# Kernel optimization log

Hardware: AMD Instinct MI355X
Metric: run time of the kernel (lower is better)

## Reference

```python
import jax, jax.numpy as jnp
import numpy as np

D_MODEL = 1024
NUM_HEADS = 16
D_HEAD = D_MODEL // NUM_HEADS
LN_EPS = 1e-5


def setup_inputs() -> dict:
    key = jax.random.key(0)
    ks = jax.random.split(key, 10)
    s = 1.0 / np.sqrt(D_MODEL)
    inp = {
        "batch": jax.random.normal(ks[0], (4, 2048, D_MODEL), dtype=jnp.float32),
        "wq": jax.random.uniform(ks[1], (D_MODEL, D_MODEL), jnp.float32, -s, s),
        "bq": jax.random.uniform(ks[2], (D_MODEL,), jnp.float32, -s, s),
        "wk": jax.random.uniform(ks[3], (D_MODEL, D_MODEL), jnp.float32, -s, s),
        "bk": jax.random.uniform(ks[4], (D_MODEL,), jnp.float32, -s, s),
        "wv": jax.random.uniform(ks[5], (D_MODEL, D_MODEL), jnp.float32, -s, s),
        "bv": jax.random.uniform(ks[6], (D_MODEL,), jnp.float32, -s, s),
        "wo": jax.random.uniform(ks[7], (D_MODEL, D_MODEL), jnp.float32, -s, s),
        "bo": jax.random.uniform(ks[8], (D_MODEL,), jnp.float32, -s, s),
        "ln_g": jnp.ones((D_MODEL,), jnp.float32),
        "ln_b": jnp.zeros((D_MODEL,), jnp.float32),
    }
    return inp


def reference(batch, wq, bq, wk, bk, wv, bv, wo, bo, ln_g, ln_b):
    B, S, D = batch.shape
    # QKV projections (torch Linear: x @ W.T + b)
    q = (batch @ wq.T + bq).reshape(B, S, NUM_HEADS, D_HEAD)
    k = (batch @ wk.T + bk).reshape(B, S, NUM_HEADS, D_HEAD)
    v = (batch @ wv.T + bv).reshape(B, S, NUM_HEADS, D_HEAD)
    # attention scores [B, H, S, S]
    scores = jnp.einsum("bqhd,bkhd->bhqk", q, k) / np.sqrt(D_HEAD).astype(np.float32)
    # (original masked_fill is not in-place -> mask has no effect; omitted)
    probs = jax.nn.softmax(scores, axis=-1)
    attn = jnp.einsum("bhqk,bkhd->bqhd", probs, v).reshape(B, S, D)
    residual = attn @ wo.T + bo  # dropout = identity (eval mode)
    x = batch + residual
    mu = jnp.mean(x, axis=-1, keepdims=True)
    var = jnp.mean(jnp.square(x - mu), axis=-1, keepdims=True)
    return (x - mu) / jnp.sqrt(var + LN_EPS) * ln_g + ln_b
```

## Files before the change

### kernel.cpp

```cpp
#include <hip/hip_runtime.h>

typedef __bf16 bf16_t;
typedef __bf16 v8bf __attribute__((ext_vector_type(8)));
typedef __bf16 v4bf __attribute__((ext_vector_type(4)));
typedef float  v4f  __attribute__((ext_vector_type(4)));

#define D_MODEL 1024
#define NHEAD   16
#define DHEAD   64
#define SEQ     2048
#define BATCH   4
#define ROWS    (BATCH*SEQ)

#define GLD16(g, l) __builtin_amdgcn_global_load_lds( \
    (const __attribute__((address_space(1))) void*)(g), \
    (__attribute__((address_space(3))) void*)(l), 16, 0, 0)

__global__ __launch_bounds__(256) void k_prep(const float* __restrict__ batch,
                                              const float* __restrict__ wq,
                                              const float* __restrict__ wk,
                                              const float* __restrict__ wv,
                                              const float* __restrict__ wo,
                                              const float* __restrict__ bq,
                                              const float* __restrict__ bk,
                                              const float* __restrict__ bv,
                                              bf16_t* __restrict__ Xb,
                                              bf16_t* __restrict__ Wqkv,
                                              bf16_t* __restrict__ Wob,
                                              float* __restrict__ bqkv) {
    int bid = blockIdx.x, t = threadIdx.x;
    const float* src; bf16_t* dst; int idx;
    if (bid < 8192)       { src = batch; dst = Xb;             idx = bid * 256 + t; }
    else if (bid < 9216)  { src = wq;    dst = Wqkv;           idx = (bid - 8192) * 256 + t; }
    else if (bid < 10240) { src = wk;    dst = Wqkv + 1048576; idx = (bid - 9216) * 256 + t; }
    else if (bid < 11264) { src = wv;    dst = Wqkv + 2097152; idx = (bid - 10240) * 256 + t; }
    else if (bid < 12288) { src = wo;    dst = Wob;            idx = (bid - 11264) * 256 + t; }
    else {
        int i = (bid - 12288) * 256 + t;
        if (i < 1024) bqkv[i] = bq[i];
        else if (i < 2048) bqkv[i] = bk[i - 1024];
        else if (i < 3072) bqkv[i] = bv[i - 2048];
        return;
    }
    float4 f = ((const float4*)src)[idx];
    v4bf o;
    o[0] = (bf16_t)f.x; o[1] = (bf16_t)f.y; o[2] = (bf16_t)f.z; o[3] = (bf16_t)f.w;
    ((v4bf*)dst)[idx] = o;
}

__global__ __launch_bounds__(256, 3) void k_gemm_bt(
    const bf16_t* __restrict__ A, const bf16_t* __restrict__ Bm,
    const float* __restrict__ bias, const float* __restrict__ resid,
    bf16_t* __restrict__ Cb, float* __restrict__ Cf,
    int M, int N, int K, int qcols, float qmul)
{
    __shared__ bf16_t As[3][128 * 32];
    __shared__ bf16_t Bs[3][128 * 32];

    int nTile = N >> 7;
    int x = blockIdx.x & 7, g = blockIdx.x >> 3;
    int n_idx = g % nTile;
    int m_idx = (g / nTile) * 8 + x;
    int m0 = m_idx << 7;
    int n0 = n_idx << 7;
    int t = threadIdx.x;
    int w = t >> 6, lane = t & 63, quad = lane >> 4, ln = lane & 15;
    int wm = (w >> 1) << 6, wn = (w & 1) << 6;

    int srow = lane >> 2;
    int scol = ((lane & 3) ^ ((lane >> 3) & 3)) << 3;
    const bf16_t* Ag0 = A  + (size_t)(m0 + w * 16 +      srow) * K + scol;
    const bf16_t* Ag1 = A  + (size_t)(m0 + w * 16 + 64 + srow) * K + scol;
    const bf16_t* Bg0 = Bm + (size_t)(n0 + w * 16 +      srow) * K + scol;
    const bf16_t* Bg1 = Bm + (size_t)(n0 + w * 16 + 64 + srow) * K + scol;
    int lo0 = (w * 16) * 32, lo1 = (w * 16 + 64) * 32;

    v4f acc[4][4];
#pragma unroll
    for (int i = 0; i < 4; i++)
#pragma unroll
        for (int j = 0; j < 4; j++) acc[i][j] = (v4f){0.f, 0.f, 0.f, 0.f};

    bf16_t* aPrev = As[2]; bf16_t* aCur = As[0]; bf16_t* aNext = As[1];
    bf16_t* bPrev = Bs[2]; bf16_t* bCur = Bs[0]; bf16_t* bNext = Bs[1];

    GLD16(Ag0, aCur + lo0);
    GLD16(Ag1, aCur + lo1);
    GLD16(Bg0, bCur + lo0);
    GLD16(Bg1, bCur + lo1);
    GLD16(Ag0 + 32, aNext + lo0);
    GLD16(Ag1 + 32, aNext + lo1);
    GLD16(Bg0 + 32, bNext + lo0);
    GLD16(Bg1 + 32, bNext + lo1);

    int sw = (ln >> 1) & 3;
    for (int k0 = 0; k0 < K; k0 += 32) {
        if (k0 + 32 < K) asm volatile("s_waitcnt vmcnt(4)" ::: "memory");
        else             asm volatile("s_waitcnt vmcnt(0)" ::: "memory");
        __builtin_amdgcn_s_barrier();
        __builtin_amdgcn_sched_barrier(0);
        if (k0 + 64 < K) {
            GLD16(Ag0 + k0 + 64, aPrev + lo0);
            GLD16(Ag1 + k0 + 64, aPrev + lo1);
            GLD16(Bg0 + k0 + 64, bPrev + lo0);
            GLD16(Bg1 + k0 + 64, bPrev + lo1);
        }
        v8bf af[4], bfr[4];
#pragma unroll
        for (int mt = 0; mt < 4; mt++)
            af[mt] = *(const v8bf*)&aCur[(wm + mt * 16 + ln) * 32 + ((quad ^ sw) << 3)];
#pragma unroll
        for (int nt = 0; nt < 4; nt++)
            bfr[nt] = *(const v8bf*)&bCur[(wn + nt * 16 + ln) * 32 + ((quad ^ sw) << 3)];
#pragma unroll
        for (int mt = 0; mt < 4; mt++)
#pragma unroll
            for (int nt = 0; nt < 4; nt++)
                acc[mt][nt] = __builtin_amdgcn_mfma_f32_16x16x32_bf16(af[mt], bfr[nt], acc[mt][nt], 0, 0, 0);
        bf16_t* ta = aPrev; aPrev = aCur; aCur = aNext; aNext = ta;
        bf16_t* tb = bPrev; bPrev = bCur; bCur = bNext; bNext = tb;
    }

#pragma unroll
    for (int mt = 0; mt < 4; mt++) {
#pragma unroll
        for (int r = 0; r < 4; r++) {
            int row = m0 + wm + mt * 16 + quad * 4 + r;
#pragma unroll
            for (int nt = 0; nt < 4; nt++) {
                int col = n0 + wn + nt * 16 + ln;
                float v = acc[mt][nt][r] + bias[col];
                if (Cf) Cf[(size_t)row * N + col] = v + resid[(size_t)row * N + col];
                else {
                    if (col < qcols) v *= qmul;
                    Cb[(size_t)row * N + col] = (bf16_t)v;
                }
            }
        }
    }
}

__global__ __launch_bounds__(256) void k_transpose_v(const bf16_t* __restrict__ qkv,
                                                     bf16_t* __restrict__ vt) {
    __shared__ bf16_t tile[64 * 72];
    int bid = blockIdx.x;
    int st = bid & 31, bh = bid >> 5, b = bh >> 4, h = bh & 15;
    int t = threadIdx.x;
    const bf16_t* src = qkv + (size_t)(b * SEQ + st * 64) * 3072 + 2048 + h * 64;
#pragma unroll
    for (int i = 0; i < 2; i++) {
        int c = t + i * 256, row = c >> 3, c8 = (c & 7) << 3;
        *(uint4*)&tile[row * 72 + c8] = *(const uint4*)(src + (size_t)row * 3072 + c8);
    }
    __syncthreads();
    bf16_t* dst = vt + (size_t)bh * DHEAD * SEQ + st * 64;
#pragma unroll
    for (int i = 0; i < 2; i++) {
        int c = t + i * 256, d = c >> 3, s8 = (c & 7) << 3;
        v8bf o;
#pragma unroll
        for (int j = 0; j < 8; j++) o[j] = tile[(s8 + j) * 72 + d];
        *(v8bf*)(dst + (size_t)d * SEQ + s8) = o;
    }
}

__global__ __launch_bounds__(256, 2) void k_attn(const bf16_t* __restrict__ qkv,
                                                 const bf16_t* __restrict__ vt,
                                                 bf16_t* __restrict__ attn) {
    __shared__ bf16_t Ks[2][64 * 64];
    __shared__ bf16_t Vs[2][64 * 64];

    int bid = blockIdx.x;
    int xcd = bid & 7, g = bid >> 3;
    int qt = g & 15;
    int bh = ((g >> 4) << 3) | xcd;
    int b = bh >> 4, h = bh & 15;
    int t = threadIdx.x, w = t >> 6, lane = t & 63, quad = lane >> 4, ln = lane & 15;
    int q0 = qt * 128 + w * 32;

    v8bf qf[2][2];
#pragma unroll
    for (int qs = 0; qs < 2; qs++) {
        const bf16_t* Qp = qkv + (size_t)(b * SEQ + q0 + qs * 16 + ln) * 3072 + h * 64 + quad * 8;
        qf[qs][0] = *(const v8bf*)Qp;
        qf[qs][1] = *(const v8bf*)(Qp + 32);
    }

    int srow = lane >> 3;
    int scol = ((lane & 7) ^ ((lane >> 3) & 3) ^ ((w & 1) << 2)) << 3;
    const bf16_t* Kg0 = qkv + (size_t)(b * SEQ + w * 8 +      srow) * 3072 + 1024 + h * 64 + scol;
    const bf16_t* Kg1 = qkv + (size_t)(b * SEQ + w * 8 + 32 + srow) * 3072 + 1024 + h * 64 + scol;
    const bf16_t* Vg0 = vt + (size_t)bh * DHEAD * SEQ + (size_t)(w * 8 +      srow) * SEQ + scol;
    const bf16_t* Vg1 = vt + (size_t)bh * DHEAD * SEQ + (size_t)(w * 8 + 32 + srow) * SEQ + scol;
    int ko0 = (w * 8) * 64, ko1 = (w * 8 + 32) * 64;

    int gk = (ln & 3) | (((ln >> 2) & 1) << 2);
    int gv = (ln & 3) | (((ln >> 3) & 1) << 2);
    int rrbase = ((ln >> 2) << 3) + (ln & 3);
    int o0 = (rrbase) * 64,       o1 = (rrbase + 4) * 64;
    int o2 = (rrbase + 32) * 64,  o3 = (rrbase + 36) * 64;

    const v4f z4 = (v4f){0.f, 0.f, 0.f, 0.f};
    v8bf ones8;
#pragma unroll
    for (int j = 0; j < 8; j++) ones8[j] = (bf16_t)1.0f;

    v4f o[2][4];
#pragma unroll
    for (int qs = 0; qs < 2; qs++)
#pragma unroll
        for (int d = 0; d < 4; d++) o[qs][d] = z4;
    v4f den[2] = {z4, z4};

    GLD16(Kg0, &Ks[0][ko0]);
    GLD16(Kg1, &Ks[0][ko1]);
    GLD16(Vg0, &Vs[0][ko0]);
    GLD16(Vg1, &Vs[0][ko1]);

    int buf = 0;
    for (int kt = 0; kt < SEQ; kt += 64, buf ^= 1) {
        __syncthreads();
        if (kt + 64 < SEQ) {
            GLD16(Kg0 + (size_t)(kt + 64) * 3072, &Ks[buf ^ 1][ko0]);
            GLD16(Kg1 + (size_t)(kt + 64) * 3072, &Ks[buf ^ 1][ko1]);
            GLD16(Vg0 + kt + 64, &Vs[buf ^ 1][ko0]);
            GLD16(Vg1 + kt + 64, &Vs[buf ^ 1][ko1]);
        }

        const bf16_t* Kb = &Ks[buf][0];
        v4f s0[4], s1[4];
        int rof[4] = {o0, o1, o2, o3};
#pragma unroll
        for (int nt = 0; nt < 4; nt++) {
            v8bf kf0 = *(const v8bf*)&Kb[rof[nt] + ((quad ^ gk) << 3)];
            v8bf kf1 = *(const v8bf*)&Kb[rof[nt] + (((quad | 4) ^ gk) << 3)];
            s0[nt] = __builtin_amdgcn_mfma_f32_16x16x32_bf16(kf0, qf[0][0], z4, 0, 0, 0);
            s0[nt] = __builtin_amdgcn_mfma_f32_16x16x32_bf16(kf1, qf[0][1], s0[nt], 0, 0, 0);
            s1[nt] = __builtin_amdgcn_mfma_f32_16x16x32_bf16(kf0, qf[1][0], z4, 0, 0, 0);
            s1[nt] = __builtin_amdgcn_mfma_f32_16x16x32_bf16(kf1, qf[1][1], s1[nt], 0, 0, 0);
        }

#pragma unroll
        for (int tk = 0; tk < 2; tk++) {
            v8bf vfd[4];
#pragma unroll
            for (int d = 0; d < 4; d++)
                vfd[d] = *(const v8bf*)&Vs[buf][(d * 16 + ln) * 64 + (((tk * 4 + quad) ^ gv) << 3)];
#pragma unroll
            for (int qs = 0; qs < 2; qs++) {
                v4f* s = qs ? s1 : s0;
                float e0 = __builtin_amdgcn_exp2f(s[2 * tk][0]);
                float e1 = __builtin_amdgcn_exp2f(s[2 * tk][1]);
                float e2 = __builtin_amdgcn_exp2f(s[2 * tk][2]);
                float e3 = __builtin_amdgcn_exp2f(s[2 * tk][3]);
                float e4 = __builtin_amdgcn_exp2f(s[2 * tk + 1][0]);
                float e5 = __builtin_amdgcn_exp2f(s[2 * tk + 1][1]);
                float e6 = __builtin_amdgcn_exp2f(s[2 * tk + 1][2]);
                float e7 = __builtin_amdgcn_exp2f(s[2 * tk + 1][3]);
                v8bf pf;
                pf[0] = (bf16_t)e0; pf[1] = (bf16_t)e1; pf[2] = (bf16_t)e2; pf[3] = (bf16_t)e3;
                pf[4] = (bf16_t)e4; pf[5] = (bf16_t)e5; pf[6] = (bf16_t)e6; pf[7] = (bf16_t)e7;
                den[qs] = __builtin_amdgcn_mfma_f32_16x16x32_bf16(pf, ones8, den[qs], 0, 0, 0);
#pragma unroll
                for (int d = 0; d < 4; d++)
                    o[qs][d] = __builtin_amdgcn_mfma_f32_16x16x32_bf16(pf, vfd[d], o[qs][d], 0, 0, 0);
            }
        }
    }

#pragma unroll
    for (int qs = 0; qs < 2; qs++) {
        int rowg = b * SEQ + q0 + qs * 16;
#pragma unroll
        for (int r = 0; r < 4; r++) {
            float inv = 1.f / den[qs][r];
#pragma unroll
            for (int d = 0; d < 4; d++)
                attn[(size_t)(rowg + quad * 4 + r) * D_MODEL + h * 64 + d * 16 + ln] =
                    (bf16_t)(o[qs][d][r] * inv);
        }
    }
}

__global__ __launch_bounds__(256) void k_layernorm(const float* __restrict__ y,
                                                   const float* __restrict__ g,
                                                   const float* __restrict__ beta,
                                                   float* __restrict__ out) {
    __shared__ float rs[4], rq[4];
    int row = blockIdx.x, t = threadIdx.x;
    int w = t >> 6, lane = t & 63;
    float4 v = ((const float4*)(y + (size_t)row * D_MODEL))[t];
    float s = v.x + v.y + v.z + v.w;
    float q = v.x * v.x + v.y * v.y + v.z * v.z + v.w * v.w;
#pragma unroll
    for (int off = 1; off < 64; off <<= 1) {
        s += __shfl_xor(s, off);
        q += __shfl_xor(q, off);
    }
    if (lane == 0) { rs[w] = s; rq[w] = q; }
    __syncthreads();
    s = rs[0] + rs[1] + rs[2] + rs[3];
    q = rq[0] + rq[1] + rq[2] + rq[3];
    float mu = s * (1.f / D_MODEL);
    float var = q * (1.f / D_MODEL) - mu * mu;
    float rstd = rsqrtf(var + 1e-5f);
    float4 gg = ((const float4*)g)[t];
    float4 bb = ((const float4*)beta)[t];
    float4 o;
    o.x = (v.x - mu) * rstd * gg.x + bb.x;
    o.y = (v.y - mu) * rstd * gg.y + bb.y;
    o.z = (v.z - mu) * rstd * gg.z + bb.z;
    o.w = (v.w - mu) * rstd * gg.w + bb.w;
    ((float4*)(out + (size_t)row * D_MODEL))[t] = o;
}

extern "C" void kernel_launch(void* const* d_in, const int* in_sizes, int n_in,
                              void* d_out, int out_size, void* d_ws, size_t ws_size,
                              hipStream_t stream) {
    const float* batch = (const float*)d_in[0];
    const float* wq = (const float*)d_in[1];
    const float* bq = (const float*)d_in[2];
    const float* wk = (const float*)d_in[3];
    const float* bk = (const float*)d_in[4];
    const float* wv = (const float*)d_in[5];
    const float* bv = (const float*)d_in[6];
    const float* wo = (const float*)d_in[7];
    const float* bo = (const float*)d_in[8];
    const float* ln_g = (const float*)d_in[9];
    const float* ln_b = (const float*)d_in[10];
    float* out = (float*)d_out;

    char* ws = (char*)d_ws;
    size_t offXb   = 0;
    size_t offWqkv = offXb + (size_t)ROWS * D_MODEL * 2;
    size_t offWo   = offWqkv + (size_t)3072 * 1024 * 2;
    size_t offBias = offWo + (size_t)1024 * 1024 * 2;
    size_t offQKV  = offBias + 3072 * 4;
    size_t offAttn = offQKV + (size_t)ROWS * 3072 * 2;
    size_t total   = offAttn + (size_t)ROWS * D_MODEL * 2;
    if (ws_size < total) return;

    bf16_t* Xb   = (bf16_t*)(ws + offXb);
    bf16_t* Vt   = (bf16_t*)(ws + offXb);
    bf16_t* Wqkv = (bf16_t*)(ws + offWqkv);
    bf16_t* Wob  = (bf16_t*)(ws + offWo);
    float*  bqkv = (float*)(ws + offBias);
    bf16_t* qkv  = (bf16_t*)(ws + offQKV);
    float*  y    = (float*)(ws + offQKV);
    bf16_t* attn = (bf16_t*)(ws + offAttn);

    const float SC = 0.125f * 1.44269504088896f;

    k_prep<<<12300, 256, 0, stream>>>(batch, wq, wk, wv, wo, bq, bk, bv,
                                      Xb, Wqkv, Wob, bqkv);
    k_gemm_bt<<<64 * 24, 256, 0, stream>>>(Xb, Wqkv, bqkv, nullptr, qkv, nullptr,
                                           8192, 3072, 1024, 1024, SC);
    k_transpose_v<<<2048, 256, 0, stream>>>(qkv, Vt);
    k_attn<<<1024, 256, 0, stream>>>(qkv, Vt, attn);
    k_gemm_bt<<<64 * 8, 256, 0, stream>>>(attn, Wob, bo, batch, nullptr, y,
                                          8192, 1024, 1024, 0, 1.0f);
    k_layernorm<<<8192, 256, 0, stream>>>(y, ln_g, ln_b, out);
}
```

Baseline: 298.4 us.

## Use 256x256-tile 8-wave pipelined GEMM for QKV projection

Replaces the 128x128-tile QKV GEMM with a dedicated 512-thread kernel that computes 256x256 output tiles. It uses double-buffered LDS split into K-halves, direct global-to-LDS loads with manual vmcnt waits and barriers, and s_setprio around the MFMA bursts. The block index is also remapped so blocks are grouped for L2 reuse. The aim is more operand reuse per LDS byte and better overlap of loads with MFMA. In exchange it has far more accumulator registers per thread, only 384 blocks, and a fragile hand-written wait schedule.

```diff
diff --git a/kernel.cpp b/kernel.cpp
--- a/kernel.cpp
+++ b/kernel.cpp
@@ -15,6 +15,15 @@
 #define GLD16(g, l) __builtin_amdgcn_global_load_lds( \
     (const __attribute__((address_space(1))) void*)(g), \
     (__attribute__((address_space(3))) void*)(l), 16, 0, 0)
+
+#define BAR asm volatile("s_barrier" ::: "memory")
+#define VW8 asm volatile("s_waitcnt vmcnt(8)" ::: "memory")
+#define VW4 asm volatile("s_waitcnt vmcnt(4)" ::: "memory")
+#define VW0 asm volatile("s_waitcnt vmcnt(0)" ::: "memory")
+#define TB   BAR
+#define TW8  do { VW8; BAR; } while(0)
+#define TW4  do { VW4; BAR; } while(0)
+#define TW0  do { VW0; BAR; } while(0)
 
 __global__ __launch_bounds__(256) void k_prep(const float* __restrict__ batch,
                                               const float* __restrict__ wq,
@@ -48,6 +57,131 @@
     ((v4bf*)dst)[idx] = o;
 }
 
+__global__ __launch_bounds__(512, 2) void k_gemm256(
+    const bf16_t* __restrict__ A, const bf16_t* __restrict__ Bm,
+    const float* __restrict__ bias, bf16_t* __restrict__ C, float qmul)
+{
+    __shared__ bf16_t As[2][2][256 * 32];
+    __shared__ bf16_t Bs[2][2][256 * 32];
+
+    const int K = 1024;
+    int bid = blockIdx.x;
+    int wg = (bid & 7) * 48 + (bid >> 3);
+    int m_idx = wg / 12, n_idx = wg % 12;
+    int m0 = m_idx << 8, n0 = n_idx << 8;
+
+    int t = threadIdx.x;
+    int lane = t & 63, quad = lane >> 4, ln = lane & 15;
+    int w = t >> 6, wr = w >> 2, wc = w & 3;
+
+    int cl = (t & 3) ^ ((t >> 2) & 3);
+    const bf16_t* Ag = A  + (size_t)(m0 + (t >> 2)) * K + cl * 8;
+    const bf16_t* Bg = Bm + (size_t)(n0 + (t >> 2)) * K + cl * 8;
+    int wb = (t >> 6) << 9;
+
+#define STA_(bufv, khv, kc) do { const bf16_t* g_ = Ag + (kc) + ((khv) << 5); \
+    GLD16(g_, &As[bufv][khv][wb]); GLD16(g_ + 131072, &As[bufv][khv][wb + 4096]); } while(0)
+#define STB_(bufv, khv, kc) do { const bf16_t* g_ = Bg + (kc) + ((khv) << 5); \
+    GLD16(g_, &Bs[bufv][khv][wb]); GLD16(g_ + 131072, &Bs[bufv][khv][wb + 4096]); } while(0)
+
+    int rsw = (quad ^ (ln & 3)) << 3;
+    int aof = (wr * 128 + ln) * 32 + rsw;
+    int bof = (wc * 64 + ln) * 32 + rsw;
+
+    v4f acc[8][4];
+#pragma unroll
+    for (int i = 0; i < 8; i++)
+#pragma unroll
+        for (int j = 0; j < 4; j++) acc[i][j] = (v4f){0.f, 0.f, 0.f, 0.f};
+
+    v8bf bfr[4];
+
+#define MFMA16(M0) \
+    acc[(M0)+0][0] = __builtin_amdgcn_mfma_f32_16x16x32_bf16(a0_, bfr[0], acc[(M0)+0][0], 0, 0, 0); \
+    acc[(M0)+0][1] = __builtin_amdgcn_mfma_f32_16x16x32_bf16(a0_, bfr[1], acc[(M0)+0][1], 0, 0, 0); \
+    acc[(M0)+0][2] = __builtin_amdgcn_mfma_f32_16x16x32_bf16(a0_, bfr[2], acc[(M0)+0][2], 0, 0, 0); \
+    acc[(M0)+0][3] = __builtin_amdgcn_mfma_f32_16x16x32_bf16(a0_, bfr[3], acc[(M0)+0][3], 0, 0, 0); \
+    acc[(M0)+1][0] = __builtin_amdgcn_mfma_f32_16x16x32_bf16(a1_, bfr[0], acc[(M0)+1][0], 0, 0, 0); \
+    acc[(M0)+1][1] = __builtin_amdgcn_mfma_f32_16x16x32_bf16(a1_, bfr[1], acc[(M0)+1][1], 0, 0, 0); \
+    acc[(M0)+1][2] = __builtin_amdgcn_mfma_f32_16x16x32_bf16(a1_, bfr[2], acc[(M0)+1][2], 0, 0, 0); \
+    acc[(M0)+1][3] = __builtin_amdgcn_mfma_f32_16x16x32_bf16(a1_, bfr[3], acc[(M0)+1][3], 0, 0, 0); \
+    acc[(M0)+2][0] = __builtin_amdgcn_mfma_f32_16x16x32_bf16(a2_, bfr[0], acc[(M0)+2][0], 0, 0, 0); \
+    acc[(M0)+2][1] = __builtin_amdgcn_mfma_f32_16x16x32_bf16(a2_, bfr[1], acc[(M0)+2][1], 0, 0, 0); \
+    acc[(M0)+2][2] = __builtin_amdgcn_mfma_f32_16x16x32_bf16(a2_, bfr[2], acc[(M0)+2][2], 0, 0, 0); \
+    acc[(M0)+2][3] = __builtin_amdgcn_mfma_f32_16x16x32_bf16(a2_, bfr[3], acc[(M0)+2][3], 0, 0, 0); \
+    acc[(M0)+3][0] = __builtin_amdgcn_mfma_f32_16x16x32_bf16(a3_, bfr[0], acc[(M0)+3][0], 0, 0, 0); \
+    acc[(M0)+3][1] = __builtin_amdgcn_mfma_f32_16x16x32_bf16(a3_, bfr[1], acc[(M0)+3][1], 0, 0, 0); \
+    acc[(M0)+3][2] = __builtin_amdgcn_mfma_f32_16x16x32_bf16(a3_, bfr[2], acc[(M0)+3][2], 0, 0, 0); \
+    acc[(M0)+3][3] = __builtin_amdgcn_mfma_f32_16x16x32_bf16(a3_, bfr[3], acc[(M0)+3][3], 0, 0, 0);
+
+#define PHASE(bufv, khv, mhv, STAGE, TAIL) do { \
+    const bf16_t* Ab_ = &As[bufv][khv][0]; \
+    if (!(mhv)) { \
+        const bf16_t* Bb_ = &Bs[bufv][khv][0]; \
+        bfr[0] = *(const v8bf*)&Bb_[bof]; \
+        bfr[1] = *(const v8bf*)&Bb_[bof + 512]; \
+        bfr[2] = *(const v8bf*)&Bb_[bof + 1024]; \
+        bfr[3] = *(const v8bf*)&Bb_[bof + 1536]; \
+    } \
+    v8bf a0_ = *(const v8bf*)&Ab_[aof + ((mhv) * 4 + 0) * 512]; \
+    v8bf a1_ = *(const v8bf*)&Ab_[aof + ((mhv) * 4 + 1) * 512]; \
+    v8bf a2_ = *(const v8bf*)&Ab_[aof + ((mhv) * 4 + 2) * 512]; \
+    v8bf a3_ = *(const v8bf*)&Ab_[aof + ((mhv) * 4 + 3) * 512]; \
+    STAGE; \
+    BAR; \
+    __builtin_amdgcn_s_setprio(1); \
+    MFMA16((mhv) * 4); \
+    __builtin_amdgcn_s_setprio(0); \
+    TAIL; \
+} while(0)
+
+    STA_(0, 0, 0); STB_(0, 0, 0);
+    STA_(0, 1, 0); STB_(0, 1, 0);
+    STA_(1, 0, 64); STB_(1, 0, 64);
+    VW8; BAR;
+
+    int kb = 0;
+#pragma unroll 1
+    for (int tp = 0; tp < 7; ++tp, kb += 128) {
+        PHASE(0, 0, 0, STA_(1, 1, kb + 64),  TB);
+        PHASE(0, 0, 1, STB_(1, 1, kb + 64),  TW8);
+        PHASE(0, 1, 0, STA_(0, 0, kb + 128), TB);
+        PHASE(0, 1, 1, STB_(0, 0, kb + 128), TW8);
+        PHASE(1, 0, 0, STA_(0, 1, kb + 128), TB);
+        PHASE(1, 0, 1, STB_(0, 1, kb + 128), TW8);
+        PHASE(1, 1, 0, STA_(1, 0, kb + 192), TB);
+        PHASE(1, 1, 1, STB_(1, 0, kb + 192), TW8);
+    }
+    PHASE(0, 0, 0, STA_(1, 1, 960), TB);
+    PHASE(0, 0, 1, STB_(1, 1, 960), TW8);
+    PHASE(0, 1, 0, ((void)0),       TB);
+    PHASE(0, 1, 1, ((void)0),       TW4);
+    PHASE(1, 0, 0, ((void)0), TB);
+    PHASE(1, 0, 1, ((void)0), TW0);
+    PHASE(1, 1, 0, ((void)0), TB);
+    PHASE(1, 1, 1, ((void)0), TB);
+
+#undef PHASE
+#undef MFMA16
+#undef STA_
+#undef STB_
+
+#pragma unroll
+    for (int m = 0; m < 8; m++) {
+#pragma unroll
+        for (int r = 0; r < 4; r++) {
+            int row = m0 + wr * 128 + m * 16 + quad * 4 + r;
+#pragma unroll
+            for (int n = 0; n < 4; n++) {
+                int col = n0 + wc * 64 + n * 16 + ln;
+                float v = acc[m][n][r] + bias[col];
+                if (col < 1024) v *= qmul;
+                C[(size_t)row * 3072 + col] = (bf16_t)v;
+            }
+        }
+    }
+}
+
 __global__ __launch_bounds__(256, 3) void k_gemm_bt(
     const bf16_t* __restrict__ A, const bf16_t* __restrict__ Bm,
     const float* __restrict__ bias, const float* __restrict__ resid,
@@ -353,8 +487,7 @@
 
     k_prep<<<12300, 256, 0, stream>>>(batch, wq, wk, wv, wo, bq, bk, bv,
                                       Xb, Wqkv, Wob, bqkv);
-    k_gemm_bt<<<64 * 24, 256, 0, stream>>>(Xb, Wqkv, bqkv, nullptr, qkv, nullptr,
-                                           8192, 3072, 1024, 1024, SC);
+    k_gemm256<<<384, 512, 0, stream>>>(Xb, Wqkv, bqkv, qkv, SC);
     k_transpose_v<<<2048, 256, 0, stream>>>(qkv, Vt);
     k_attn<<<1024, 256, 0, stream>>>(qkv, Vt, attn);
     k_gemm_bt<<<64 * 8, 256, 0, stream>>>(attn, Wob, bo, batch, nullptr, y,
```

New measurement: 303.1 us. Within noise of the previous version (+1.6%).

## Use 128x256 tile GEMM for QKV projection and re-swizzle V LDS layout

Applied to the files above, without the earlier changes.

Adds a new GEMM kernel with 128x256 output tiles (each wave computes 64x128) and an XCD-aware block mapping, used for the fused QKV projection. The wider tile raises arithmetic intensity and cuts re-reads of A from global memory, but uses more accumulator registers and LDS, so occupancy drops to 2 blocks per CU. The attention kernel also switches to a different XOR swizzle for V tiles in LDS, which is meant to reduce bank conflicts on the V reads. The epilogue writes scalar bf16 stores, which are less coalesced than vector stores.

```diff
diff --git a/kernel.cpp b/kernel.cpp
--- a/kernel.cpp
+++ b/kernel.cpp
@@ -48,6 +48,98 @@
     ((v4bf*)dst)[idx] = o;
 }
 
+__global__ __launch_bounds__(256, 2) void k_gemm_bt2(
+    const bf16_t* __restrict__ A, const bf16_t* __restrict__ Bm,
+    const float* __restrict__ bias, bf16_t* __restrict__ Cb,
+    int M, int N, int K, int qcols, float qmul)
+{
+    __shared__ bf16_t As[3][128 * 32];
+    __shared__ bf16_t Bs[3][256 * 32];
+
+    int nT = N >> 8;
+    int cpx = ((M >> 7) * nT) >> 3;
+    int bid = blockIdx.x;
+    int wg = (bid & 7) * cpx + (bid >> 3);
+    int m_idx = wg / nT, n_idx = wg % nT;
+    int m0 = m_idx << 7, n0 = n_idx << 8;
+
+    int t = threadIdx.x;
+    int w = t >> 6, lane = t & 63, quad = lane >> 4, ln = lane & 15;
+    int wm = (w >> 1) << 6, wn = (w & 1) << 7;
+
+    int srow = lane >> 2;
+    int scol = ((lane & 3) ^ ((lane >> 3) & 3)) << 3;
+    const bf16_t* Ag0 = A  + (size_t)(m0 + w * 16 + srow) * K + scol;
+    const bf16_t* Ag1 = Ag0 + (size_t)64 * K;
+    const bf16_t* Bg0 = Bm + (size_t)(n0 + w * 16 + srow) * K + scol;
+    const bf16_t* Bg1 = Bg0 + (size_t)64 * K;
+    const bf16_t* Bg2 = Bg0 + (size_t)128 * K;
+    const bf16_t* Bg3 = Bg0 + (size_t)192 * K;
+    int la0 = (w * 16) * 32, la1 = (w * 16 + 64) * 32;
+    int lb0 = (w * 16) * 32;
+
+    v4f acc[4][8];
+#pragma unroll
+    for (int i = 0; i < 4; i++)
+#pragma unroll
+        for (int j = 0; j < 8; j++) acc[i][j] = (v4f){0.f, 0.f, 0.f, 0.f};
+
+    bf16_t* aPrev = As[2]; bf16_t* aCur = As[0]; bf16_t* aNext = As[1];
+    bf16_t* bPrev = Bs[2]; bf16_t* bCur = Bs[0]; bf16_t* bNext = Bs[1];
+
+    GLD16(Ag0, aCur + la0); GLD16(Ag1, aCur + la1);
+    GLD16(Bg0, bCur + lb0); GLD16(Bg1, bCur + lb0 + 2048);
+    GLD16(Bg2, bCur + lb0 + 4096); GLD16(Bg3, bCur + lb0 + 6144);
+    GLD16(Ag0 + 32, aNext + la0); GLD16(Ag1 + 32, aNext + la1);
+    GLD16(Bg0 + 32, bNext + lb0); GLD16(Bg1 + 32, bNext + lb0 + 2048);
+    GLD16(Bg2 + 32, bNext + lb0 + 4096); GLD16(Bg3 + 32, bNext + lb0 + 6144);
+
+    int rsw = (quad ^ ((ln >> 1) & 3)) << 3;
+    for (int k0 = 0; k0 < K; k0 += 32) {
+        if (k0 + 32 < K) asm volatile("s_waitcnt vmcnt(6)" ::: "memory");
+        else             asm volatile("s_waitcnt vmcnt(0)" ::: "memory");
+        __builtin_amdgcn_s_barrier();
+        __builtin_amdgcn_sched_barrier(0);
+        if (k0 + 64 < K) {
+            GLD16(Ag0 + k0 + 64, aPrev + la0);
+            GLD16(Ag1 + k0 + 64, aPrev + la1);
+            GLD16(Bg0 + k0 + 64, bPrev + lb0);
+            GLD16(Bg1 + k0 + 64, bPrev + lb0 + 2048);
+            GLD16(Bg2 + k0 + 64, bPrev + lb0 + 4096);
+            GLD16(Bg3 + k0 + 64, bPrev + lb0 + 6144);
+        }
+        v8bf af[4], bfr[8];
+#pragma unroll
+        for (int mt = 0; mt < 4; mt++)
+            af[mt] = *(const v8bf*)&aCur[(wm + mt * 16 + ln) * 32 + rsw];
+#pragma unroll
+        for (int nt = 0; nt < 8; nt++)
+            bfr[nt] = *(const v8bf*)&bCur[(wn + nt * 16 + ln) * 32 + rsw];
+#pragma unroll
+        for (int mt = 0; mt < 4; mt++)
+#pragma unroll
+            for (int nt = 0; nt < 8; nt++)
+                acc[mt][nt] = __builtin_amdgcn_mfma_f32_16x16x32_bf16(af[mt], bfr[nt], acc[mt][nt], 0, 0, 0);
+        bf16_t* ta = aPrev; aPrev = aCur; aCur = aNext; aNext = ta;
+        bf16_t* tb = bPrev; bPrev = bCur; bCur = bNext; bNext = tb;
+    }
+
+#pragma unroll
+    for (int mt = 0; mt < 4; mt++) {
+#pragma unroll
+        for (int r = 0; r < 4; r++) {
+            int row = m0 + wm + mt * 16 + quad * 4 + r;
+#pragma unroll
+            for (int nt = 0; nt < 8; nt++) {
+                int col = n0 + wn + nt * 16 + ln;
+                float v = acc[mt][nt][r] + bias[col];
+                if (col < qcols) v *= qmul;
+                Cb[(size_t)row * N + col] = (bf16_t)v;
+            }
+        }
+    }
+}
+
 __global__ __launch_bounds__(256, 3) void k_gemm_bt(
     const bf16_t* __restrict__ A, const bf16_t* __restrict__ Bm,
     const float* __restrict__ bias, const float* __restrict__ resid,
@@ -187,15 +279,16 @@
     }
 
     int srow = lane >> 3;
-    int scol = ((lane & 7) ^ ((lane >> 3) & 3) ^ ((w & 1) << 2)) << 3;
-    const bf16_t* Kg0 = qkv + (size_t)(b * SEQ + w * 8 +      srow) * 3072 + 1024 + h * 64 + scol;
-    const bf16_t* Kg1 = qkv + (size_t)(b * SEQ + w * 8 + 32 + srow) * 3072 + 1024 + h * 64 + scol;
-    const bf16_t* Vg0 = vt + (size_t)bh * DHEAD * SEQ + (size_t)(w * 8 +      srow) * SEQ + scol;
-    const bf16_t* Vg1 = vt + (size_t)bh * DHEAD * SEQ + (size_t)(w * 8 + 32 + srow) * SEQ + scol;
+    int scolK = ((lane & 7) ^ ((lane >> 3) & 3) ^ ((w & 1) << 2)) << 3;
+    int scolV = ((lane & 7) ^ (lane >> 3)) << 3;
+    const bf16_t* Kg0 = qkv + (size_t)(b * SEQ + w * 8 +      srow) * 3072 + 1024 + h * 64 + scolK;
+    const bf16_t* Kg1 = qkv + (size_t)(b * SEQ + w * 8 + 32 + srow) * 3072 + 1024 + h * 64 + scolK;
+    const bf16_t* Vg0 = vt + (size_t)bh * DHEAD * SEQ + (size_t)(w * 8 +      srow) * SEQ + scolV;
+    const bf16_t* Vg1 = vt + (size_t)bh * DHEAD * SEQ + (size_t)(w * 8 + 32 + srow) * SEQ + scolV;
     int ko0 = (w * 8) * 64, ko1 = (w * 8 + 32) * 64;
 
     int gk = (ln & 3) | (((ln >> 2) & 1) << 2);
-    int gv = (ln & 3) | (((ln >> 3) & 1) << 2);
+    int gv = ln & 7;
     int rrbase = ((ln >> 2) << 3) + (ln & 3);
     int o0 = (rrbase) * 64,       o1 = (rrbase + 4) * 64;
     int o2 = (rrbase + 32) * 64,  o3 = (rrbase + 36) * 64;
@@ -353,8 +446,8 @@
 
     k_prep<<<12300, 256, 0, stream>>>(batch, wq, wk, wv, wo, bq, bk, bv,
                                       Xb, Wqkv, Wob, bqkv);
-    k_gemm_bt<<<64 * 24, 256, 0, stream>>>(Xb, Wqkv, bqkv, nullptr, qkv, nullptr,
-                                           8192, 3072, 1024, 1024, SC);
+    k_gemm_bt2<<<768, 256, 0, stream>>>(Xb, Wqkv, bqkv, qkv,
+                                        8192, 3072, 1024, 1024, SC);
     k_transpose_v<<<2048, 256, 0, stream>>>(qkv, Vt);
     k_attn<<<1024, 256, 0, stream>>>(qkv, Vt, attn);
     k_gemm_bt<<<64 * 8, 256, 0, stream>>>(attn, Wob, bo, batch, nullptr, y,
```

After: 309.8 us. +3.8%, slower.

## Add 256x256-tile ping-pong QKV GEMM kernel and retune V LDS swizzle

Applied to the files above, without the earlier changes.

Replaces the 128x128 QKV projection GEMM with a new 512-thread kernel using 256x256 output tiles, double-buffered split-K LDS stages loaded via global_load_lds, explicit vmcnt waits, barriers and MFMA priority hints. The larger tile is meant to raise arithmetic intensity and reduce global traffic, and the software pipelining is meant to overlap loads with MFMA work. It also changes the V-tile LDS swizzle in attention to a different XOR pattern to reduce bank conflicts. The cost is higher register and LDS pressure and only 384 blocks, which may underfill the GPU.

```diff
diff --git a/kernel.cpp b/kernel.cpp
--- a/kernel.cpp
+++ b/kernel.cpp
@@ -15,6 +15,8 @@
 #define GLD16(g, l) __builtin_amdgcn_global_load_lds( \
     (const __attribute__((address_space(1))) void*)(g), \
     (__attribute__((address_space(3))) void*)(l), 16, 0, 0)
+
+#define BAR asm volatile("s_barrier" ::: "memory")
 
 __global__ __launch_bounds__(256) void k_prep(const float* __restrict__ batch,
                                               const float* __restrict__ wq,
@@ -48,6 +50,143 @@
     ((v4bf*)dst)[idx] = o;
 }
 
+__global__ __launch_bounds__(512, 2) void k_gemm256(
+    const bf16_t* __restrict__ A, const bf16_t* __restrict__ Bm,
+    const float* __restrict__ bias, bf16_t* __restrict__ C, float qmul)
+{
+    __shared__ bf16_t As[2][2][256 * 32];
+    __shared__ bf16_t Bs[2][2][256 * 32];
+
+    const int K = 1024;
+    int bid = blockIdx.x;
+    int wg = (bid & 7) * 48 + (bid >> 3);
+    int m_idx = wg / 12, n_idx = wg % 12;
+    int m0 = m_idx << 8, n0 = n_idx << 8;
+
+    int t = threadIdx.x;
+    int lane = t & 63, quad = lane >> 4, ln = lane & 15;
+    int w = t >> 6, wr = w >> 2, wc = w & 3;
+
+    int cl = (t & 3) ^ ((t >> 3) & 3);
+    const bf16_t* Ag = A  + (size_t)(m0 + (t >> 2)) * K + cl * 8;
+    const bf16_t* Bg = Bm + (size_t)(n0 + (t >> 2)) * K + cl * 8;
+    int wb = w << 9;
+
+#define STA(bufv, khv, kc) { const bf16_t* g_ = Ag + (kc) + ((khv) << 5); \
+    GLD16(g_, &As[bufv][khv][wb]); GLD16(g_ + 131072, &As[bufv][khv][wb + 4096]); }
+#define STB(bufv, khv, kc) { const bf16_t* g_ = Bg + (kc) + ((khv) << 5); \
+    GLD16(g_, &Bs[bufv][khv][wb]); GLD16(g_ + 131072, &Bs[bufv][khv][wb + 4096]); }
+
+    int rsw = (quad ^ ((ln >> 1) & 3)) << 3;
+    int aofs = (wr * 128 + ln) * 32 + rsw;
+    int bofs = (wc * 64 + ln) * 32 + rsw;
+
+#define LDA(dst, bufv, mhv) { \
+    dst[0] = *(const v8bf*)&AB_[aofs + (mhv) * 2048]; \
+    dst[1] = *(const v8bf*)&AB_[aofs + (mhv) * 2048 + 512]; \
+    dst[2] = *(const v8bf*)&AB_[aofs + (mhv) * 2048 + 1024]; \
+    dst[3] = *(const v8bf*)&AB_[aofs + (mhv) * 2048 + 1536]; }
+#define LDAF(dst, bufv, khv, mhv) { const bf16_t* AB_ = &As[bufv][khv][0]; LDA(dst, bufv, mhv) }
+#define LDBF(dst, bufv, khv) { const bf16_t* BB_ = &Bs[bufv][khv][0]; \
+    dst[0] = *(const v8bf*)&BB_[bofs]; \
+    dst[1] = *(const v8bf*)&BB_[bofs + 512]; \
+    dst[2] = *(const v8bf*)&BB_[bofs + 1024]; \
+    dst[3] = *(const v8bf*)&BB_[bofs + 1536]; }
+
+    v4f acc[8][4];
+#pragma unroll
+    for (int i = 0; i < 8; i++)
+#pragma unroll
+        for (int j = 0; j < 4; j++) acc[i][j] = (v4f){0.f, 0.f, 0.f, 0.f};
+
+    v8bf aX[4], aY[4], bX[4], bY[4];
+
+#define MF(AC, BC, M0) \
+    __builtin_amdgcn_s_setprio(1); \
+    acc[(M0)+0][0] = __builtin_amdgcn_mfma_f32_16x16x32_bf16(AC[0], BC[0], acc[(M0)+0][0], 0, 0, 0); \
+    acc[(M0)+0][1] = __builtin_amdgcn_mfma_f32_16x16x32_bf16(AC[0], BC[1], acc[(M0)+0][1], 0, 0, 0); \
+    acc[(M0)+0][2] = __builtin_amdgcn_mfma_f32_16x16x32_bf16(AC[0], BC[2], acc[(M0)+0][2], 0, 0, 0); \
+    acc[(M0)+0][3] = __builtin_amdgcn_mfma_f32_16x16x32_bf16(AC[0], BC[3], acc[(M0)+0][3], 0, 0, 0); \
+    acc[(M0)+1][0] = __builtin_amdgcn_mfma_f32_16x16x32_bf16(AC[1], BC[0], acc[(M0)+1][0], 0, 0, 0); \
+    acc[(M0)+1][1] = __builtin_amdgcn_mfma_f32_16x16x32_bf16(AC[1], BC[1], acc[(M0)+1][1], 0, 0, 0); \
+    acc[(M0)+1][2] = __builtin_amdgcn_mfma_f32_16x16x32_bf16(AC[1], BC[2], acc[(M0)+1][2], 0, 0, 0); \
+    acc[(M0)+1][3] = __builtin_amdgcn_mfma_f32_16x16x32_bf16(AC[1], BC[3], acc[(M0)+1][3], 0, 0, 0); \
+    acc[(M0)+2][0] = __builtin_amdgcn_mfma_f32_16x16x32_bf16(AC[2], BC[0], acc[(M0)+2][0], 0, 0, 0); \
+    acc[(M0)+2][1] = __builtin_amdgcn_mfma_f32_16x16x32_bf16(AC[2], BC[1], acc[(M0)+2][1], 0, 0, 0); \
+    acc[(M0)+2][2] = __builtin_amdgcn_mfma_f32_16x16x32_bf16(AC[2], BC[2], acc[(M0)+2][2], 0, 0, 0); \
+    acc[(M0)+2][3] = __builtin_amdgcn_mfma_f32_16x16x32_bf16(AC[2], BC[3], acc[(M0)+2][3], 0, 0, 0); \
+    acc[(M0)+3][0] = __builtin_amdgcn_mfma_f32_16x16x32_bf16(AC[3], BC[0], acc[(M0)+3][0], 0, 0, 0); \
+    acc[(M0)+3][1] = __builtin_amdgcn_mfma_f32_16x16x32_bf16(AC[3], BC[1], acc[(M0)+3][1], 0, 0, 0); \
+    acc[(M0)+3][2] = __builtin_amdgcn_mfma_f32_16x16x32_bf16(AC[3], BC[2], acc[(M0)+3][2], 0, 0, 0); \
+    acc[(M0)+3][3] = __builtin_amdgcn_mfma_f32_16x16x32_bf16(AC[3], BC[3], acc[(M0)+3][3], 0, 0, 0); \
+    __builtin_amdgcn_s_setprio(0);
+
+#define TAIL_W6 { asm volatile("s_waitcnt vmcnt(6)" ::: "memory"); BAR; __builtin_amdgcn_sched_barrier(0); }
+#define TAIL_W4 { asm volatile("s_waitcnt vmcnt(4)" ::: "memory"); BAR; __builtin_amdgcn_sched_barrier(0); }
+#define TAIL_W0 { asm volatile("s_waitcnt vmcnt(0)" ::: "memory"); BAR; __builtin_amdgcn_sched_barrier(0); }
+#define TAIL_B  { BAR; __builtin_amdgcn_sched_barrier(0); }
+
+    STA(0, 0, 0); STB(0, 0, 0);
+    STA(0, 1, 0); STB(0, 1, 0);
+    STA(1, 0, 64); STB(1, 0, 64);
+    asm volatile("s_waitcnt vmcnt(8)" ::: "memory");
+    BAR; __builtin_amdgcn_sched_barrier(0);
+    LDAF(aX, 0, 0, 0); LDBF(bX, 0, 0);
+
+#define TILE(b, kc, S1, S2, S3, S4, T1, T3, P4B, P4LD) \
+    S1; LDAF(aY, b, 0, 1);                    MF(aX, bX, 0); T1; \
+    S2; LDBF(bY, b, 1); LDAF(aX, b, 1, 0);    MF(aY, bX, 4); TAIL_B; \
+    S3; LDAF(aY, b, 1, 1);                    MF(aX, bY, 0); T3; \
+    S4; if (P4LD) { LDBF(bX, P4B, 0); LDAF(aX, P4B, 0, 0); } \
+                                              MF(aY, bY, 4); TAIL_B;
+
+    int kb = 0;
+#pragma unroll 1
+    for (int tp = 0; tp < 7; ++tp, kb += 128) {
+        TILE(0, kb, STA(1, 1, kb + 64), STB(1, 1, kb + 64),
+                    STA(0, 0, kb + 128), STB(0, 0, kb + 128),
+                    TAIL_W6, TAIL_W6, 1, 1)
+        TILE(1, kb + 64, STA(0, 1, kb + 128), STB(0, 1, kb + 128),
+                         STA(1, 0, kb + 192), STB(1, 0, kb + 192),
+                         TAIL_W6, TAIL_W6, 0, 1)
+    }
+    TILE(0, 896, STA(1, 1, 960), STB(1, 1, 960), , ,
+                 TAIL_W6, TAIL_W4, 1, 1)
+    { const int b = 1;
+      LDAF(aY, b, 0, 1);                    MF(aX, bX, 0); TAIL_W0;
+      LDBF(bY, b, 1); LDAF(aX, b, 1, 0);    MF(aY, bX, 4); TAIL_B;
+      LDAF(aY, b, 1, 1);                    MF(aX, bY, 0); TAIL_B;
+                                            MF(aY, bY, 4);
+    }
+
+#undef TILE
+#undef MF
+#undef TAIL_W6
+#undef TAIL_W4
+#undef TAIL_W0
+#undef TAIL_B
+#undef LDA
+#undef LDAF
+#undef LDBF
+#undef STA
+#undef STB
+
+#pragma unroll
+    for (int m = 0; m < 8; m++) {
+#pragma unroll
+        for (int r = 0; r < 4; r++) {
+            int row = m0 + wr * 128 + m * 16 + quad * 4 + r;
+#pragma unroll
+            for (int n = 0; n < 4; n++) {
+                int col = n0 + wc * 64 + n * 16 + ln;
+                float v = acc[m][n][r] + bias[col];
+                if (col < 1024) v *= qmul;
+                C[(size_t)row * 3072 + col] = (bf16_t)v;
+            }
+        }
+    }
+}
+
 __global__ __launch_bounds__(256, 3) void k_gemm_bt(
     const bf16_t* __restrict__ A, const bf16_t* __restrict__ Bm,
     const float* __restrict__ bias, const float* __restrict__ resid,
@@ -187,15 +326,16 @@
     }
 
     int srow = lane >> 3;
-    int scol = ((lane & 7) ^ ((lane >> 3) & 3) ^ ((w & 1) << 2)) << 3;
-    const bf16_t* Kg0 = qkv + (size_t)(b * SEQ + w * 8 +      srow) * 3072 + 1024 + h * 64 + scol;
-    const bf16_t* Kg1 = qkv + (size_t)(b * SEQ + w * 8 + 32 + srow) * 3072 + 1024 + h * 64 + scol;
-    const bf16_t* Vg0 = vt + (size_t)bh * DHEAD * SEQ + (size_t)(w * 8 +      srow) * SEQ + scol;
-    const bf16_t* Vg1 = vt + (size_t)bh * DHEAD * SEQ + (size_t)(w * 8 + 32 + srow) * SEQ + scol;
+    int scolK = ((lane & 7) ^ ((lane >> 3) & 3) ^ ((w & 1) << 2)) << 3;
+    int scolV = ((lane & 7) ^ (lane >> 3)) << 3;
+    const bf16_t* Kg0 = qkv + (size_t)(b * SEQ + w * 8 +      srow) * 3072 + 1024 + h * 64 + scolK;
+    const bf16_t* Kg1 = qkv + (size_t)(b * SEQ + w * 8 + 32 + srow) * 3072 + 1024 + h * 64 + scolK;
+    const bf16_t* Vg0 = vt + (size_t)bh * DHEAD * SEQ + (size_t)(w * 8 +      srow) * SEQ + scolV;
+    const bf16_t* Vg1 = vt + (size_t)bh * DHEAD * SEQ + (size_t)(w * 8 + 32 + srow) * SEQ + scolV;
     int ko0 = (w * 8) * 64, ko1 = (w * 8 + 32) * 64;
 
     int gk = (ln & 3) | (((ln >> 2) & 1) << 2);
-    int gv = (ln & 3) | (((ln >> 3) & 1) << 2);
+    int gv = ln & 7;
     int rrbase = ((ln >> 2) << 3) + (ln & 3);
     int o0 = (rrbase) * 64,       o1 = (rrbase + 4) * 64;
     int o2 = (rrbase + 32) * 64,  o3 = (rrbase + 36) * 64;
@@ -353,8 +493,7 @@
 
     k_prep<<<12300, 256, 0, stream>>>(batch, wq, wk, wv, wo, bq, bk, bv,
                                       Xb, Wqkv, Wob, bqkv);
-    k_gemm_bt<<<64 * 24, 256, 0, stream>>>(Xb, Wqkv, bqkv, nullptr, qkv, nullptr,
-                                           8192, 3072, 1024, 1024, SC);
+    k_gemm256<<<384, 512, 0, stream>>>(Xb, Wqkv, bqkv, qkv, SC);
     k_transpose_v<<<2048, 256, 0, stream>>>(qkv, Vt);
     k_attn<<<1024, 256, 0, stream>>>(qkv, Vt, attn);
     k_gemm_bt<<<64 * 8, 256, 0, stream>>>(attn, Wob, bo, batch, nullptr, y,
```

New measurement: 304.2 us. About the same (+1.9%).
